# Performance work log

Hardware: AMD Instinct MI355X
Metric: run time of the kernel (lower is better)

Reference implementation:

```python
import jax, jax.numpy as jnp
import numpy as np

B, T, DEPTH, VOCAB, NCHILD = 2, 256, 8, 32000, 64


def setup_inputs() -> dict:
    key = jax.random.key(0)
    k1, k2, k3, k4 = jax.random.split(key, 4)
    child_tokens = jax.random.randint(k1, (B, T, DEPTH, NCHILD), 0, VOCAB, dtype=jnp.int32)
    child_counts = jax.random.uniform(k2, (B, T, DEPTH, NCHILD), dtype=jnp.float32) * 100.0
    w = jax.random.normal(k3, (DEPTH,), dtype=jnp.float32) * 0.02  # Linear(depth, 1) weight
    bias = jax.random.normal(k4, (1,), dtype=jnp.float32) * 0.02
    return {"child_tokens": child_tokens, "child_counts": child_counts, "w": w, "bias": bias}


def reference(child_tokens, child_counts, w, bias):
    b, t, depth, nchild = child_tokens.shape
    # Scatter per-node child counts into ml_input[b, t, depth, vocab]
    bi = jnp.arange(b)[:, None, None, None]
    ti = jnp.arange(t)[None, :, None, None]
    di = jnp.arange(depth)[None, None, :, None]
    ml_input = jnp.zeros((b, t, depth, VOCAB), dtype=child_counts.dtype)
    ml_input = ml_input.at[bi, ti, di, child_tokens].add(child_counts)
    # transpose(2,3) -> [b, t, vocab, depth]; Linear(depth -> 1); squeeze
    out = jnp.einsum('btdv,d->btv', ml_input, w) + bias[0]
    return out  # [b, t, vocab]
```

## Files before the change

kernel.cpp:

```cpp
#include <hip/hip_runtime.h>


#define BB 2
#define TT 256
#define DEPTHD 8
#define VOCABV 32000
#define NCHILDC 64

__global__ void tt_fill_bias(float* __restrict__ out,
                             const float* __restrict__ bias, int n4) {
    float b = bias[0];
    float4 v = make_float4(b, b, b, b);
    float4* __restrict__ o = reinterpret_cast<float4*>(out);
    int idx = blockIdx.x * blockDim.x + threadIdx.x;
    int stride = gridDim.x * blockDim.x;
    for (int i = idx; i < n4; i += stride) {
        o[i] = v;
    }
}

__global__ void tt_scatter_add(const int* __restrict__ tokens,
                               const float* __restrict__ counts,
                               const float* __restrict__ w,
                               float* __restrict__ out) {
    int i = blockIdx.x * blockDim.x + threadIdx.x;
    int d   = (i >> 6) & 7;
    int row = i >> 9;
    int tok = tokens[i];
    float val = counts[i] * w[d];
    atomicAdd(out + (long)row * VOCABV + tok, val);
}

extern "C" void kernel_launch(void* const* d_in, const int* in_sizes, int n_in,
                              void* d_out, int out_size, void* d_ws, size_t ws_size,
                              hipStream_t stream) {
    const int*   tokens = (const int*)d_in[0];
    const float* counts = (const float*)d_in[1];
    const float* w      = (const float*)d_in[2];
    const float* bias   = (const float*)d_in[3];
    float* out = (float*)d_out;

    int n4 = out_size / 4;
    tt_fill_bias<<<2048, 256, 0, stream>>>(out, bias, n4);

    int total = BB * TT * DEPTHD * NCHILDC;
    tt_scatter_add<<<total / 256, 256, 0, stream>>>(tokens, counts, w, out);
}
```

Before: 96.11 us.

## Fuse bias fill and scatter-add into one LDS-accumulating kernel per half-row

Measured after the change: 82.36 us. 14.3% less time.

```diff
diff --git a/kernel.cpp b/kernel.cpp
--- a/kernel.cpp
+++ b/kernel.cpp
@@ -6,29 +6,45 @@
 #define DEPTHD 8
 #define VOCABV 32000
 #define NCHILDC 64
+#define HALF (VOCABV / 2)
+#define ENTRIES (DEPTHD * NCHILDC)
 
-__global__ void tt_fill_bias(float* __restrict__ out,
-                             const float* __restrict__ bias, int n4) {
-    float b = bias[0];
-    float4 v = make_float4(b, b, b, b);
-    float4* __restrict__ o = reinterpret_cast<float4*>(out);
-    int idx = blockIdx.x * blockDim.x + threadIdx.x;
-    int stride = gridDim.x * blockDim.x;
-    for (int i = idx; i < n4; i += stride) {
-        o[i] = v;
+__global__ __launch_bounds__(1024, 1) void tt_fused(
+    const int* __restrict__ tokens,
+    const float* __restrict__ counts,
+    const float* __restrict__ w,
+    const float* __restrict__ bias,
+    float* __restrict__ out)
+{
+    __shared__ float acc[HALF];
+    const int bid  = blockIdx.x;
+    const int row  = bid >> 1;
+    const int half = bid & 1;
+    const int tid  = threadIdx.x;
+
+    float4* acc4 = reinterpret_cast<float4*>(acc);
+    #pragma unroll
+    for (int i = tid; i < HALF / 4; i += 1024)
+        acc4[i] = make_float4(0.f, 0.f, 0.f, 0.f);
+    __syncthreads();
+
+    if (tid < ENTRIES) {
+        const int idx = row * ENTRIES + tid;
+        const int tok = tokens[idx];
+        const float val = counts[idx] * w[(tid >> 6) & 7];
+        const int local = tok - half * HALF;
+        if ((unsigned)local < (unsigned)HALF)
+            atomicAdd(&acc[local], val);
     }
-}
+    __syncthreads();
 
-__global__ void tt_scatter_add(const int* __restrict__ tokens,
-                               const float* __restrict__ counts,
-                               const float* __restrict__ w,
-                               float* __restrict__ out) {
-    int i = blockIdx.x * blockDim.x + threadIdx.x;
-    int d   = (i >> 6) & 7;
-    int row = i >> 9;
-    int tok = tokens[i];
-    float val = counts[i] * w[d];
-    atomicAdd(out + (long)row * VOCABV + tok, val);
+    const float b = bias[0];
+    float4* o4 = reinterpret_cast<float4*>(out + (size_t)row * VOCABV + half * HALF);
+    #pragma unroll
+    for (int i = tid; i < HALF / 4; i += 1024) {
+        float4 v = acc4[i];
+        o4[i] = make_float4(v.x + b, v.y + b, v.z + b, v.w + b);
+    }
 }
 
 extern "C" void kernel_launch(void* const* d_in, const int* in_sizes, int n_in,
@@ -40,9 +56,6 @@
     const float* bias   = (const float*)d_in[3];
     float* out = (float*)d_out;
 
-    int n4 = out_size / 4;
-    tt_fill_bias<<<2048, 256, 0, stream>>>(out, bias, n4);
-
-    int total = BB * TT * DEPTHD * NCHILDC;
-    tt_scatter_add<<<total / 256, 256, 0, stream>>>(tokens, counts, w, out);
+    const int nblocks = BB * TT * 2;
+    tt_fused<<<nblocks, 1024, 0, stream>>>(tokens, counts, w, bias, out);
 }
```
